# Kernel optimization log

Hardware: AMD Instinct MI355X
Metric: run time of the kernel (lower is better)

Reference implementation:

```python
import jax, jax.numpy as jnp
import numpy as np

GROUPS = 32  # from analyze_enhance_linear_ops(4096, 4096, 0.05): smallest divisor g with 1/g <= 0.05


def setup_inputs() -> dict:
    key = jax.random.key(0)
    k1, k2, k3, k4, k5 = jax.random.split(key, 5)
    B, S, D_in, D_out = 4, 2048, 4096, 4096
    ig = D_out // GROUPS  # 128
    x = jax.random.normal(k1, (B, S, D_in), dtype=jnp.float32)
    W = jax.random.normal(k2, (D_out, D_in), dtype=jnp.float32) * 0.02
    b = jax.random.normal(k3, (D_out,), dtype=jnp.float32) * 0.02
    Wg = jax.random.normal(k4, (GROUPS, ig, ig), dtype=jnp.float32) * 0.02
    bg = jax.random.normal(k5, (GROUPS, ig), dtype=jnp.float32) * 0.02
    return {"x": x, "W": W, "b": b, "Wg": Wg, "bg": bg}


def reference(x, W, b, Wg, bg):
    # original_linear: dense GEMM, torch Linear layout W[out, in]
    y = jnp.einsum('bsi,oi->bso', x, W) + b            # [B, S, D_out]
    # GroupedLinear: block-diagonal transform over groups of size out_group
    B, S, D = y.shape
    G, og, ig = Wg.shape
    yg = y.reshape(B, S, G, ig)                        # split into groups
    out = jnp.einsum('bsgi,goi->bsgo', yg, Wg) + bg    # per-group small GEMM + bias
    return out.reshape(B, S, D)                        # cat along feature dim
```

## Files before the change

### kernel.cpp

```cpp
#include <hip/hip_runtime.h>
#include <hip/hip_bf16.h>
#include <stdint.h>

typedef float f32x4 __attribute__((ext_vector_type(4)));
typedef short s16x8 __attribute__((ext_vector_type(8)));
typedef unsigned int u32x2 __attribute__((ext_vector_type(2)));
typedef unsigned int u32x4 __attribute__((ext_vector_type(4)));

#define MDIM 8192
#define NDIM 4096
#define KDIM 4096
#define NKT  64

__device__ __forceinline__ unsigned pkbf(float lo, float hi) {
  unsigned short l = __builtin_bit_cast(unsigned short, __float2bfloat16(lo));
  unsigned short h = __builtin_bit_cast(unsigned short, __float2bfloat16(hi));
  return ((unsigned)h << 16) | (unsigned)l;
}

__device__ __forceinline__ void gload16(const void* g, void* l) {
  __builtin_amdgcn_global_load_lds((const __attribute__((address_space(1))) int*)g,
                                   (__attribute__((address_space(3))) int*)l, 16, 0, 0);
}

__global__ __launch_bounds__(256) void conv_tile(
    const float* __restrict__ X, const float* __restrict__ W,
    s16x8* __restrict__ wsA, s16x8* __restrict__ wsB) {
  __shared__ char lds[32768];
  const int b = blockIdx.x;
  const float* src;
  s16x8* dst;
  int bi;
  if (b < 32 * NKT) { src = X; dst = wsA; bi = b; }
  else              { src = W; dst = wsB; bi = b - 32 * NKT; }
  const int rt = bi >> 6;
  const int kt = bi & 63;
  const int tid = threadIdx.x;
  const int fr = tid >> 4;
  const int c4 = (tid & 15) * 4;
  const int h = c4 >> 5, q = (c4 >> 3) & 3, eh = (c4 >> 2) & 1;
  #pragma unroll
  for (int f = 0; f < 16; ++f) {
    const int row = f * 16 + fr;
    f32x4 v = *(const f32x4*)(src + ((size_t)rt * 256 + row) * KDIM + kt * 64 + c4);
    u32x2 p = { pkbf(v[0], v[1]), pkbf(v[2], v[3]) };
    *(u32x2*)(lds + (h * 16 + f) * 1024 + (q * 16 + fr) * 16 + eh * 8) = p;
  }
  __syncthreads();
  const size_t ob = (size_t)bi * 2048;
  #pragma unroll
  for (int i = 0; i < 8; ++i)
    dst[ob + i * 256 + tid] = *(const s16x8*)(lds + (i * 256 + tid) * 16);
}

__global__ __launch_bounds__(512, 2) void gemm256(
    const s16x8* __restrict__ wsA, const s16x8* __restrict__ wsB,
    const float* __restrict__ bias, const float* __restrict__ Wg,
    const float* __restrict__ bg, float* __restrict__ out) {
  extern __shared__ char smem[];
  const int tid = threadIdx.x;
  const int lane = tid & 63;
  const int wid = tid >> 6;
  const int wr = wid >> 2;
  const int wc = wid & 3;
  const int fr = lane & 15;
  const int q4 = lane >> 4;

  const int bid = blockIdx.x;
  const int swz = (bid & 7) * 64 + (bid >> 3);
  const int bm = swz >> 4;
  const int bn = swz & 15;

  const size_t aBase = (size_t)bm * NKT * 2048;
  const size_t bBase = (size_t)bn * NKT * 2048;

  auto stage = [&](int kt, int db, int isB, int h) {
    const s16x8* s = (isB ? wsB + bBase : wsA + aBase)
                     + (size_t)kt * 2048 + h * 1024 + wid * 128 + lane;
    char* d = smem + isB * 65536 + db * 32768 + h * 16384 + wid * 2048;
    gload16(s, d);
    gload16(s + 64, d + 1024);
  };

  const char* aRd = smem + wr * 8192 + lane * 16;
  const char* bRd = smem + 65536 + wc * 4096 + lane * 16;

  f32x4 acc[8][4];
  #pragma unroll
  for (int m = 0; m < 8; ++m)
    #pragma unroll
    for (int n = 0; n < 4; ++n) acc[m][n] = (f32x4)0.0f;

  s16x8 af[8], bfr[2];

#define PHASE(DB, H, NH, SKT, SDB, SOP, SH, DOVM)                              \
  {                                                                            \
    if ((NH) == 0) {                                                           \
      _Pragma("unroll")                                                        \
      for (int m = 0; m < 8; ++m)                                              \
        af[m] = *(const s16x8*)(aRd + (DB)*32768 + (H)*16384 + m * 1024);      \
    }                                                                          \
    bfr[0] = *(const s16x8*)(bRd + (DB)*32768 + (H)*16384 + (NH)*2048);        \
    bfr[1] = *(const s16x8*)(bRd + (DB)*32768 + (H)*16384 + (NH)*2048 + 1024); \
    stage(SKT, SDB, SOP, SH);                                                  \
    if (DOVM) asm volatile("s_waitcnt vmcnt(6)" ::: "memory");                 \
    __builtin_amdgcn_s_barrier();                                              \
    asm volatile("s_waitcnt lgkmcnt(0)" ::: "memory");                         \
    __builtin_amdgcn_s_setprio(1);                                             \
    _Pragma("unroll")                                                          \
    for (int m = 0; m < 8; ++m) {                                              \
      acc[m][(NH)*2] = __builtin_amdgcn_mfma_f32_16x16x32_bf16(                \
          af[m], bfr[0], acc[m][(NH)*2], 0, 0, 0);                             \
      acc[m][(NH)*2 + 1] = __builtin_amdgcn_mfma_f32_16x16x32_bf16(            \
          af[m], bfr[1], acc[m][(NH)*2 + 1], 0, 0, 0);                         \
    }                                                                          \
    __builtin_amdgcn_s_setprio(0);                                             \
    __builtin_amdgcn_s_barrier();                                              \
  }

  stage(0, 0, 0, 0); stage(0, 0, 1, 0); stage(0, 0, 0, 1); stage(0, 0, 1, 1);
  stage(1, 1, 0, 0); stage(1, 1, 1, 0); stage(1, 1, 0, 1);
  asm volatile("s_waitcnt vmcnt(6)" ::: "memory");
  __builtin_amdgcn_s_barrier();

  for (int it = 0; it < 32; ++it) {
    const int u0 = 2 * it;
    const int k1 = u0 + 1;
    const int k2 = (u0 + 2 < NKT) ? u0 + 2 : NKT - 1;
    const int k3 = (u0 + 3 < NKT) ? u0 + 3 : NKT - 1;
    PHASE(0, 0, 0, k1, 1, 1, 1, 0)
    PHASE(0, 0, 1, k2, 0, 0, 0, 0)
    PHASE(0, 1, 0, k2, 0, 1, 0, 0)
    PHASE(0, 1, 1, k2, 0, 0, 1, 1)
    PHASE(1, 0, 0, k2, 0, 1, 1, 0)
    PHASE(1, 0, 1, k3, 1, 0, 0, 0)
    PHASE(1, 1, 0, k3, 1, 1, 0, 0)
    PHASE(1, 1, 1, k3, 1, 0, 1, 1)
  }
#undef PHASE

  asm volatile("s_waitcnt vmcnt(0)" ::: "memory");
  __builtin_amdgcn_s_barrier();

  float bv[4];
  #pragma unroll
  for (int n = 0; n < 4; ++n) bv[n] = bias[bn * 256 + wc * 64 + n * 16 + fr];

  #pragma unroll
  for (int m = 0; m < 8; ++m) {
    #pragma unroll
    for (int n = 0; n < 4; ++n) {
      const int Kh = wc * 2 + (n >> 1);
      const int qq = (n & 1) * 2 + (fr >> 3);
      const int Mf = wr * 8 + m;
      #pragma unroll
      for (int r = 0; r < 4; ++r) {
        const int frs = q4 * 4 + r;
        const float y = acc[m][n][r] + bv[n];
        *(unsigned short*)(smem + (Mf * 8 + Kh) * 1024 + (qq * 16 + frs) * 16 + (fr & 7) * 2)
            = __builtin_bit_cast(unsigned short, __float2bfloat16(y));
      }
    }
  }
  asm volatile("s_waitcnt lgkmcnt(0)" ::: "memory");
  __builtin_amdgcn_s_barrier();

  const int g = bn * 2 + (wc >> 1);
  const float* wgb = Wg + (size_t)g * 16384;
  f32x4 acc2[8][4];
  #pragma unroll
  for (int m = 0; m < 8; ++m)
    #pragma unroll
    for (int n = 0; n < 4; ++n) acc2[m][n] = (f32x4)0.0f;

  #pragma unroll
  for (int s = 0; s < 4; ++s) {
    const int Kh = (wc >> 1) * 4 + s;
    s16x8 af2[8];
    #pragma unroll
    for (int m = 0; m < 8; ++m)
      af2[m] = *(const s16x8*)(smem + ((wr * 8 + m) * 8 + Kh) * 1024 + lane * 16);
    #pragma unroll
    for (int n = 0; n < 4; ++n) {
      const int ocl = (wc & 1) * 64 + n * 16 + fr;
      const float* wp = wgb + ocl * 128 + s * 32 + q4 * 8;
      f32x4 w0 = *(const f32x4*)wp;
      f32x4 w1 = *(const f32x4*)(wp + 4);
      u32x4 pw = { pkbf(w0[0], w0[1]), pkbf(w0[2], w0[3]),
                   pkbf(w1[0], w1[1]), pkbf(w1[2], w1[3]) };
      const s16x8 bfw = __builtin_bit_cast(s16x8, pw);
      #pragma unroll
      for (int m = 0; m < 8; ++m)
        acc2[m][n] = __builtin_amdgcn_mfma_f32_16x16x32_bf16(af2[m], bfw, acc2[m][n], 0, 0, 0);
    }
  }

  float bgv[4];
  #pragma unroll
  for (int n = 0; n < 4; ++n) bgv[n] = bg[bn * 256 + wc * 64 + n * 16 + fr];

  #pragma unroll
  for (int m = 0; m < 8; ++m) {
    #pragma unroll
    for (int n = 0; n < 4; ++n) {
      const int col = bn * 256 + wc * 64 + n * 16 + fr;
      #pragma unroll
      for (int r = 0; r < 4; ++r) {
        const size_t row = (size_t)bm * 256 + wr * 128 + m * 16 + q4 * 4 + r;
        out[row * NDIM + col] = acc2[m][n][r] + bgv[n];
      }
    }
  }
}

extern "C" void kernel_launch(void* const* d_in, const int* in_sizes, int n_in,
                              void* d_out, int out_size, void* d_ws, size_t ws_size,
                              hipStream_t stream) {
  const float* X    = (const float*)d_in[0];
  const float* W    = (const float*)d_in[1];
  const float* bias = (const float*)d_in[2];
  const float* Wg   = (const float*)d_in[3];
  const float* bg   = (const float*)d_in[4];
  float* out = (float*)d_out;

  s16x8* wsA = (s16x8*)d_ws;
  s16x8* wsB = wsA + ((size_t)MDIM * KDIM / 8);

  static int lds_attr_set = 0;
  (void)lds_attr_set;
  hipFuncSetAttribute(reinterpret_cast<const void*>(gemm256),
                      hipFuncAttributeMaxDynamicSharedMemorySize, 131072);

  conv_tile<<<dim3(32 * NKT + 16 * NKT), dim3(256), 0, stream>>>(X, W, wsA, wsB);
  gemm256<<<dim3(512), dim3(512), 131072, stream>>>(wsA, wsB, bias, Wg, bg, out);
}
```

Baseline: 293.2 us.

## Split GEMM phases by M-halves with four B fragments and reorder epilogue stores

Each pipeline phase now loads four B fragments once per k-half and four A fragments per M-half, instead of eight A fragments plus two B fragments per N-half. This rebalances LDS reads against MFMAs and moves the global-to-LDS stage issue to the start of each phase. The stage schedule and the initial vmcnt wait are adjusted to match. The bias-add epilogue now rotates the register index by q4 when writing bf16 values to LDS, which should reduce bank conflicts. The reordered staging carries a risk of wrong wait counts or races if the new order does not line up with the loads.

```diff
diff --git a/kernel.cpp b/kernel.cpp
--- a/kernel.cpp
+++ b/kernel.cpp
@@ -28,6 +28,7 @@
     s16x8* __restrict__ wsA, s16x8* __restrict__ wsB) {
   __shared__ char lds[32768];
   const int b = blockIdx.x;
+  const int tid = threadIdx.x;
   const float* src;
   s16x8* dst;
   int bi;
@@ -35,7 +36,6 @@
   else              { src = W; dst = wsB; bi = b - 32 * NKT; }
   const int rt = bi >> 6;
   const int kt = bi & 63;
-  const int tid = threadIdx.x;
   const int fr = tid >> 4;
   const int c4 = (tid & 15) * 4;
   const int h = c4 >> 5, q = (c4 >> 3) & 3, eh = (c4 >> 2) & 1;
@@ -91,36 +91,37 @@
     #pragma unroll
     for (int n = 0; n < 4; ++n) acc[m][n] = (f32x4)0.0f;
 
-  s16x8 af[8], bfr[2];
-
-#define PHASE(DB, H, NH, SKT, SDB, SOP, SH, DOVM)                              \
+  s16x8 af[4], bfr[4];
+
+#define PHASE(DB, H, MH, SKT, SDB, SOP, SH, DOVM)                              \
   {                                                                            \
-    if ((NH) == 0) {                                                           \
+    stage(SKT, SDB, SOP, SH);                                                  \
+    if ((MH) == 0) {                                                           \
       _Pragma("unroll")                                                        \
-      for (int m = 0; m < 8; ++m)                                              \
-        af[m] = *(const s16x8*)(aRd + (DB)*32768 + (H)*16384 + m * 1024);      \
+      for (int n = 0; n < 4; ++n)                                              \
+        bfr[n] = *(const s16x8*)(bRd + (DB)*32768 + (H)*16384 + n * 1024);     \
     }                                                                          \
-    bfr[0] = *(const s16x8*)(bRd + (DB)*32768 + (H)*16384 + (NH)*2048);        \
-    bfr[1] = *(const s16x8*)(bRd + (DB)*32768 + (H)*16384 + (NH)*2048 + 1024); \
-    stage(SKT, SDB, SOP, SH);                                                  \
+    _Pragma("unroll")                                                          \
+    for (int m = 0; m < 4; ++m)                                                \
+      af[m] = *(const s16x8*)(aRd + (DB)*32768 + (H)*16384 + ((MH)*4 + m) * 1024); \
     if (DOVM) asm volatile("s_waitcnt vmcnt(6)" ::: "memory");                 \
     __builtin_amdgcn_s_barrier();                                              \
     asm volatile("s_waitcnt lgkmcnt(0)" ::: "memory");                         \
     __builtin_amdgcn_s_setprio(1);                                             \
     _Pragma("unroll")                                                          \
-    for (int m = 0; m < 8; ++m) {                                              \
-      acc[m][(NH)*2] = __builtin_amdgcn_mfma_f32_16x16x32_bf16(                \
-          af[m], bfr[0], acc[m][(NH)*2], 0, 0, 0);                             \
-      acc[m][(NH)*2 + 1] = __builtin_amdgcn_mfma_f32_16x16x32_bf16(            \
-          af[m], bfr[1], acc[m][(NH)*2 + 1], 0, 0, 0);                         \
+    for (int m = 0; m < 4; ++m) {                                              \
+      _Pragma("unroll")                                                        \
+      for (int n = 0; n < 4; ++n)                                              \
+        acc[(MH)*4 + m][n] = __builtin_amdgcn_mfma_f32_16x16x32_bf16(          \
+            af[m], bfr[n], acc[(MH)*4 + m][n], 0, 0, 0);                       \
     }                                                                          \
     __builtin_amdgcn_s_setprio(0);                                             \
     __builtin_amdgcn_s_barrier();                                              \
   }
 
   stage(0, 0, 0, 0); stage(0, 0, 1, 0); stage(0, 0, 0, 1); stage(0, 0, 1, 1);
-  stage(1, 1, 0, 0); stage(1, 1, 1, 0); stage(1, 1, 0, 1);
-  asm volatile("s_waitcnt vmcnt(6)" ::: "memory");
+  stage(1, 1, 0, 0); stage(1, 1, 1, 0); stage(1, 1, 1, 1);
+  asm volatile("s_waitcnt vmcnt(3)" ::: "memory");
   __builtin_amdgcn_s_barrier();
 
   for (int it = 0; it < 32; ++it) {
@@ -128,14 +129,14 @@
     const int k1 = u0 + 1;
     const int k2 = (u0 + 2 < NKT) ? u0 + 2 : NKT - 1;
     const int k3 = (u0 + 3 < NKT) ? u0 + 3 : NKT - 1;
-    PHASE(0, 0, 0, k1, 1, 1, 1, 0)
-    PHASE(0, 0, 1, k2, 0, 0, 0, 0)
-    PHASE(0, 1, 0, k2, 0, 1, 0, 0)
-    PHASE(0, 1, 1, k2, 0, 0, 1, 1)
-    PHASE(1, 0, 0, k2, 0, 1, 1, 0)
-    PHASE(1, 0, 1, k3, 1, 0, 0, 0)
-    PHASE(1, 1, 0, k3, 1, 1, 0, 0)
-    PHASE(1, 1, 1, k3, 1, 0, 1, 1)
+    PHASE(0, 0, 0, k1, 1, 0, 1, 0)
+    PHASE(0, 0, 1, k2, 0, 1, 0, 0)
+    PHASE(0, 1, 0, k2, 0, 0, 0, 0)
+    PHASE(0, 1, 1, k2, 0, 1, 1, 1)
+    PHASE(1, 0, 0, k2, 0, 0, 1, 0)
+    PHASE(1, 0, 1, k3, 1, 1, 0, 0)
+    PHASE(1, 1, 0, k3, 1, 0, 0, 0)
+    PHASE(1, 1, 1, k3, 1, 1, 1, 1)
   }
 #undef PHASE
 
@@ -148,15 +149,17 @@
 
   #pragma unroll
   for (int m = 0; m < 8; ++m) {
-    #pragma unroll
-    for (int n = 0; n < 4; ++n) {
-      const int Kh = wc * 2 + (n >> 1);
-      const int qq = (n & 1) * 2 + (fr >> 3);
-      const int Mf = wr * 8 + m;
+    const int Mf = wr * 8 + m;
+    #pragma unroll
+    for (int np = 0; np < 2; ++np) {
+      const int Kh = wc * 2 + np;
       #pragma unroll
-      for (int r = 0; r < 4; ++r) {
+      for (int j = 0; j < 8; ++j) {
+        const int nn = np * 2 + (j >> 2);
+        const int r = (j + q4) & 3;
+        const int qq = (j >> 2) * 2 + (fr >> 3);
         const int frs = q4 * 4 + r;
-        const float y = acc[m][n][r] + bv[n];
+        const float y = acc[m][nn][r] + bv[nn];
         *(unsigned short*)(smem + (Mf * 8 + Kh) * 1024 + (qq * 16 + frs) * 16 + (fr & 7) * 2)
             = __builtin_bit_cast(unsigned short, __float2bfloat16(y));
       }
@@ -226,11 +229,9 @@
   s16x8* wsA = (s16x8*)d_ws;
   s16x8* wsB = wsA + ((size_t)MDIM * KDIM / 8);
 
-  static int lds_attr_set = 0;
-  (void)lds_attr_set;
   hipFuncSetAttribute(reinterpret_cast<const void*>(gemm256),
                       hipFuncAttributeMaxDynamicSharedMemorySize, 131072);
 
-  conv_tile<<<dim3(32 * NKT + 16 * NKT), dim3(256), 0, stream>>>(X, W, wsA, wsB);
+  conv_tile<<<dim3(3072), dim3(256), 0, stream>>>(X, W, wsA, wsB);
   gemm256<<<dim3(512), dim3(512), 131072, stream>>>(wsA, wsB, bias, Wg, bg, out);
 }
```

After: 298.2 us. About the same (+1.7%).
